# Performance work log

Measured on AMD Instinct MI355X. Metric: run time of the kernel, lower is better.

## Reference

```python
import jax, jax.numpy as jnp
import numpy as np

N = 50000      # nodes
E = 800000     # edges (before self-loops)
IN = 256
HID = 256
OUT = 128
D = 4
K = 4
K1 = 8
NUM_KS = K1 * ((1 << K) - 1)   # 120 centroids
S = HID // D                   # sub-dim per quantization slice
TAU = 1.0


def setup_inputs() -> dict:
    key = jax.random.key(0)
    ks = jax.random.split(key, 9)
    x = jax.random.normal(ks[0], (N, IN), jnp.float32)
    edge_index = jax.random.randint(ks[1], (2, E), 0, N, dtype=jnp.int64)
    def lin(k, fan_in, fan_out):
        return jax.random.normal(k, (fan_in, fan_out), jnp.float32) / np.float32(np.sqrt(fan_in))
    W0 = lin(ks[2], IN, HID); b0 = jnp.zeros((HID,), jnp.float32)
    W1 = lin(ks[3], HID, HID); b1 = jnp.zeros((HID,), jnp.float32)
    W2 = lin(ks[4], HID, OUT); b2 = jnp.zeros((OUT,), jnp.float32)
    # kaiming_normal on (NUM_KS, HID): std = sqrt(2 / fan_in), fan_in = HID
    centroids = jax.random.normal(ks[5], (NUM_KS, HID), jnp.float32) * np.float32(np.sqrt(2.0 / HID))
    return dict(x=x, edge_index=edge_index, W0=W0, b0=b0, W1=W1, b1=b1, W2=W2, b2=b2,
                centroids=centroids)


def gcn_conv(x, W, b, src, dst):
    # PyG GCNConv: add self-loops, symmetric normalization, aggregate at target
    n = x.shape[0]
    loops = jnp.arange(n, dtype=src.dtype)
    s2 = jnp.concatenate([src, loops])
    d2 = jnp.concatenate([dst, loops])
    deg = jax.ops.segment_sum(jnp.ones_like(d2, x.dtype), d2, num_segments=n)
    dinv = jnp.where(deg > 0, jax.lax.rsqrt(deg), 0.0)
    norm = dinv[s2] * dinv[d2]                      # [E+n]
    xw = x @ W                                      # [n, out]
    out = jax.ops.segment_sum(xw[s2] * norm[:, None], d2, num_segments=n)
    return out + b


def quantize(H, C):
    # H: [n, HID], C: [NUM_KS, HID]
    n = H.shape[0]
    Hr = H.reshape(n, D, S)
    Cr = C.reshape(NUM_KS, D, S)
    # products[n,k,d] = sum_s H[n,d,s] * C[k,d,s]
    prods = jnp.einsum('nds,kds->nkd', Hr, Cr) / TAU   # [n, NUM_KS, D]
    soft_l, hard_l, prob_l = [], [], []
    off = 0
    d_idx = jnp.arange(D)[None, :]
    for j in range(K):                 # K fixed small groups of sizes k_1<<j
        m = K1 << j
        sl = prods[:, off:off + m, :]                  # [n, m, D]
        p = jax.nn.softmax(sl, axis=1)                 # scatter_softmax within group
        Cg = Cr[off:off + m]                           # [m, D, S]
        soft_l.append(jnp.einsum('nmd,mds->nds', p, Cg))
        idx = jnp.argmax(sl, axis=1)                   # [n, D] scatter_max within group
        hard_l.append(Cg[idx, d_idx, :])               # [n, D, S]
        prob_l.append(p)
        off += m
    soft = jnp.stack(soft_l, 1).reshape(n, K, HID)
    hard = jnp.stack(hard_l, 1).reshape(n, K, HID)
    q = jax.lax.stop_gradient(hard - soft) + soft      # straight-through
    balance = jnp.concatenate(prob_l, 1).sum(0) / n    # [NUM_KS, D]
    k_blns = jnp.concatenate([jnp.full((K1 << j,), 1.0 / (K1 << j), jnp.float32) for j in range(K)])
    target = jnp.broadcast_to(k_blns[:, None], (NUM_KS, D))
    reg = jnp.linalg.norm(balance - target)
    pred = jnp.max(q, axis=1)                          # [n, HID]
    return pred, reg


def reference(x, edge_index, W0, b0, W1, b1, W2, b2, centroids):
    src, dst = edge_index[0], edge_index[1]
    h = jax.nn.leaky_relu(gcn_conv(x, W0, b0, src, dst), negative_slope=0.5)
    h = jax.nn.leaky_relu(gcn_conv(h, W1, b1, src, dst), negative_slope=0.5)
    pred, reg = quantize(h, centroids)
    h = h + pred
    out = gcn_conv(h, W2, b2, src, dst)
    return out, reg
```

## Files before the change

### kernel.cpp

```cpp
#include <hip/hip_runtime.h>
#include <math.h>



__global__ void k_init(int* cnt, int* cursor, int* counter, float* balance, int n) {
    int i = blockIdx.x * blockDim.x + threadIdx.x;
    if (i < n) { cnt[i] = 0; cursor[i] = 0; }
    if (i < 480) balance[i] = 0.f;
    if (i == 0) *counter = 0;
}

__global__ void k_count(const int* __restrict__ dst, int* __restrict__ cnt, int e) {
    int i = blockIdx.x * blockDim.x + threadIdx.x;
    if (i < e) atomicAdd(&cnt[dst[i]], 1);
}

__global__ void k_dinv(const int* __restrict__ cnt, float* __restrict__ dinv, int n) {
    int i = blockIdx.x * blockDim.x + threadIdx.x;
    if (i < n) dinv[i] = rsqrtf((float)cnt[i] + 1.0f);
}

__global__ void k_alloc(const int* __restrict__ cnt, int* __restrict__ row_start,
                        int* __restrict__ counter, int n) {
    int i = blockIdx.x * blockDim.x + threadIdx.x;
    if (i < n) row_start[i] = atomicAdd(counter, cnt[i]);
}

__global__ void k_fill(const int* __restrict__ src, const int* __restrict__ dst,
                       const float* __restrict__ dinv, const int* __restrict__ row_start,
                       int* __restrict__ cursor, int* __restrict__ csr_src,
                       float* __restrict__ csr_norm, int e) {
    int i = blockIdx.x * blockDim.x + threadIdx.x;
    if (i >= e) return;
    int s = src[i], d = dst[i];
    int slot = atomicAdd(&cursor[d], 1);
    int idx = row_start[d] + slot;
    csr_src[idx] = s;
    csr_norm[idx] = dinv[s] * dinv[d];
}


__global__ __launch_bounds__(256, 2) void k_gemm(const float* __restrict__ A,
                                                 const float* __restrict__ B,
                                                 float* __restrict__ C,
                                                 int M, int N, int K) {
    __shared__ float As[32][132];
    __shared__ float Bs[32][132];
    const int tid = threadIdx.x;
    const int bm = blockIdx.x * 128;
    const int bn = blockIdx.y * 128;
    const int tx = tid & 15, ty = tid >> 4;
    float acc[2][2][4][4] = {};

    for (int k0 = 0; k0 < K; k0 += 32) {
#pragma unroll
        for (int v = 0; v < 4; ++v) {
            int row = (tid >> 3) + v * 32;
            int col = (tid & 7) * 4;
            float4 a = make_float4(0.f, 0.f, 0.f, 0.f);
            if (bm + row < M) a = *(const float4*)(A + (size_t)(bm + row) * K + k0 + col);
            As[col + 0][row] = a.x;
            As[col + 1][row] = a.y;
            As[col + 2][row] = a.z;
            As[col + 3][row] = a.w;
        }
#pragma unroll
        for (int v = 0; v < 4; ++v) {
            int kr = (tid >> 5) + v * 8;
            int col = (tid & 31) * 4;
            *(float4*)&Bs[kr][col] = *(const float4*)(B + (size_t)(k0 + kr) * N + bn + col);
        }
        __syncthreads();
#pragma unroll
        for (int kk = 0; kk < 32; ++kk) {
            float4 a0 = *(float4*)&As[kk][ty * 4];
            float4 a1 = *(float4*)&As[kk][64 + ty * 4];
            float4 b0 = *(float4*)&Bs[kk][tx * 4];
            float4 b1 = *(float4*)&Bs[kk][64 + tx * 4];
            float av[2][4] = {{a0.x, a0.y, a0.z, a0.w}, {a1.x, a1.y, a1.z, a1.w}};
            float bv[2][4] = {{b0.x, b0.y, b0.z, b0.w}, {b1.x, b1.y, b1.z, b1.w}};
#pragma unroll
            for (int ri = 0; ri < 2; ++ri)
#pragma unroll
                for (int i = 0; i < 4; ++i)
#pragma unroll
                    for (int ci = 0; ci < 2; ++ci)
#pragma unroll
                        for (int j = 0; j < 4; ++j)
                            acc[ri][ci][i][j] += av[ri][i] * bv[ci][j];
        }
        __syncthreads();
    }
#pragma unroll
    for (int ri = 0; ri < 2; ++ri)
#pragma unroll
        for (int i = 0; i < 4; ++i) {
            int row = bm + ri * 64 + ty * 4 + i;
            if (row < M) {
#pragma unroll
                for (int ci = 0; ci < 2; ++ci) {
                    float4 o = make_float4(acc[ri][ci][i][0], acc[ri][ci][i][1],
                                           acc[ri][ci][i][2], acc[ri][ci][i][3]);
                    *(float4*)(C + (size_t)row * N + bn + ci * 64 + tx * 4) = o;
                }
            }
        }
}


template <bool RELU>
__global__ __launch_bounds__(256, 4) void k_agg4(const float* __restrict__ xw,
                                                 const float* __restrict__ dinv,
                                                 const int* __restrict__ csr_src,
                                                 const float* __restrict__ csr_norm,
                                                 const int* __restrict__ row_start,
                                                 const int* __restrict__ cnt,
                                                 const float* __restrict__ bias,
                                                 float* __restrict__ out, int n) {
    int node = blockIdx.x * 4 + (threadIdx.x >> 6);
    if (node >= n) return;
    int lane = threadIdx.x & 63;
    int c = lane * 4;
    float di = dinv[node];
    float4 self = *(const float4*)(xw + (size_t)node * 256 + c);
    float4 bv = *(const float4*)(bias + c);
    float sw = di * di;
    float ax = self.x * sw + bv.x;
    float ay = self.y * sw + bv.y;
    float az = self.z * sw + bv.z;
    float aw = self.w * sw + bv.w;
    int st = row_start[node];
    int m = cnt[node];
    for (int t0 = 0; t0 < m; t0 += 64) {
        int rem = m - t0;
        int cnt_i = rem < 64 ? rem : 64;
        int idx_l = 0;
        float nrm_l = 0.f;
        if (lane < cnt_i) {
            idx_l = csr_src[st + t0 + lane];
            nrm_l = csr_norm[st + t0 + lane];
        }
        int t = 0;
        for (; t + 8 <= cnt_i; t += 8) {
            const float* p0 = xw + (size_t)__shfl(idx_l, t + 0, 64) * 256 + c;
            const float* p1 = xw + (size_t)__shfl(idx_l, t + 1, 64) * 256 + c;
            const float* p2 = xw + (size_t)__shfl(idx_l, t + 2, 64) * 256 + c;
            const float* p3 = xw + (size_t)__shfl(idx_l, t + 3, 64) * 256 + c;
            const float* p4 = xw + (size_t)__shfl(idx_l, t + 4, 64) * 256 + c;
            const float* p5 = xw + (size_t)__shfl(idx_l, t + 5, 64) * 256 + c;
            const float* p6 = xw + (size_t)__shfl(idx_l, t + 6, 64) * 256 + c;
            const float* p7 = xw + (size_t)__shfl(idx_l, t + 7, 64) * 256 + c;
            float4 v0 = *(const float4*)p0;
            float4 v1 = *(const float4*)p1;
            float4 v2 = *(const float4*)p2;
            float4 v3 = *(const float4*)p3;
            float4 v4 = *(const float4*)p4;
            float4 v5 = *(const float4*)p5;
            float4 v6 = *(const float4*)p6;
            float4 v7 = *(const float4*)p7;
            float w0 = __shfl(nrm_l, t + 0, 64);
            float w1 = __shfl(nrm_l, t + 1, 64);
            float w2 = __shfl(nrm_l, t + 2, 64);
            float w3 = __shfl(nrm_l, t + 3, 64);
            float w4 = __shfl(nrm_l, t + 4, 64);
            float w5 = __shfl(nrm_l, t + 5, 64);
            float w6 = __shfl(nrm_l, t + 6, 64);
            float w7 = __shfl(nrm_l, t + 7, 64);
            ax += v0.x * w0; ay += v0.y * w0; az += v0.z * w0; aw += v0.w * w0;
            ax += v1.x * w1; ay += v1.y * w1; az += v1.z * w1; aw += v1.w * w1;
            ax += v2.x * w2; ay += v2.y * w2; az += v2.z * w2; aw += v2.w * w2;
            ax += v3.x * w3; ay += v3.y * w3; az += v3.z * w3; aw += v3.w * w3;
            ax += v4.x * w4; ay += v4.y * w4; az += v4.z * w4; aw += v4.w * w4;
            ax += v5.x * w5; ay += v5.y * w5; az += v5.z * w5; aw += v5.w * w5;
            ax += v6.x * w6; ay += v6.y * w6; az += v6.z * w6; aw += v6.w * w6;
            ax += v7.x * w7; ay += v7.y * w7; az += v7.z * w7; aw += v7.w * w7;
        }
        for (; t < cnt_i; ++t) {
            int s = __shfl(idx_l, t, 64);
            float w = __shfl(nrm_l, t, 64);
            float4 v = *(const float4*)(xw + (size_t)s * 256 + c);
            ax += v.x * w; ay += v.y * w; az += v.z * w; aw += v.w * w;
        }
    }
    if (RELU) {
        ax = ax > 0.f ? ax : 0.5f * ax;
        ay = ay > 0.f ? ay : 0.5f * ay;
        az = az > 0.f ? az : 0.5f * az;
        aw = aw > 0.f ? aw : 0.5f * aw;
    }
    *(float4*)(out + (size_t)node * 256 + c) = make_float4(ax, ay, az, aw);
}

__global__ __launch_bounds__(256, 4) void k_agg2(const float* __restrict__ xw,
                                                 const float* __restrict__ dinv,
                                                 const int* __restrict__ csr_src,
                                                 const float* __restrict__ csr_norm,
                                                 const int* __restrict__ row_start,
                                                 const int* __restrict__ cnt,
                                                 const float* __restrict__ bias,
                                                 float* __restrict__ out, int n) {
    int node = blockIdx.x * 4 + (threadIdx.x >> 6);
    if (node >= n) return;
    int lane = threadIdx.x & 63;
    int c = lane * 2;
    float di = dinv[node];
    float2 self = *(const float2*)(xw + (size_t)node * 128 + c);
    float2 bv = *(const float2*)(bias + c);
    float sw = di * di;
    float ax = self.x * sw + bv.x;
    float ay = self.y * sw + bv.y;
    int st = row_start[node];
    int m = cnt[node];
    for (int t0 = 0; t0 < m; t0 += 64) {
        int rem = m - t0;
        int cnt_i = rem < 64 ? rem : 64;
        int idx_l = 0;
        float nrm_l = 0.f;
        if (lane < cnt_i) {
            idx_l = csr_src[st + t0 + lane];
            nrm_l = csr_norm[st + t0 + lane];
        }
        int t = 0;
        for (; t + 8 <= cnt_i; t += 8) {
            const float* p0 = xw + (size_t)__shfl(idx_l, t + 0, 64) * 128 + c;
            const float* p1 = xw + (size_t)__shfl(idx_l, t + 1, 64) * 128 + c;
            const float* p2 = xw + (size_t)__shfl(idx_l, t + 2, 64) * 128 + c;
            const float* p3 = xw + (size_t)__shfl(idx_l, t + 3, 64) * 128 + c;
            const float* p4 = xw + (size_t)__shfl(idx_l, t + 4, 64) * 128 + c;
            const float* p5 = xw + (size_t)__shfl(idx_l, t + 5, 64) * 128 + c;
            const float* p6 = xw + (size_t)__shfl(idx_l, t + 6, 64) * 128 + c;
            const float* p7 = xw + (size_t)__shfl(idx_l, t + 7, 64) * 128 + c;
            float2 v0 = *(const float2*)p0;
            float2 v1 = *(const float2*)p1;
            float2 v2 = *(const float2*)p2;
            float2 v3 = *(const float2*)p3;
            float2 v4 = *(const float2*)p4;
            float2 v5 = *(const float2*)p5;
            float2 v6 = *(const float2*)p6;
            float2 v7 = *(const float2*)p7;
            float w0 = __shfl(nrm_l, t + 0, 64);
            float w1 = __shfl(nrm_l, t + 1, 64);
            float w2 = __shfl(nrm_l, t + 2, 64);
            float w3 = __shfl(nrm_l, t + 3, 64);
            float w4 = __shfl(nrm_l, t + 4, 64);
            float w5 = __shfl(nrm_l, t + 5, 64);
            float w6 = __shfl(nrm_l, t + 6, 64);
            float w7 = __shfl(nrm_l, t + 7, 64);
            ax += v0.x * w0; ay += v0.y * w0;
            ax += v1.x * w1; ay += v1.y * w1;
            ax += v2.x * w2; ay += v2.y * w2;
            ax += v3.x * w3; ay += v3.y * w3;
            ax += v4.x * w4; ay += v4.y * w4;
            ax += v5.x * w5; ay += v5.y * w5;
            ax += v6.x * w6; ay += v6.y * w6;
            ax += v7.x * w7; ay += v7.y * w7;
        }
        for (; t < cnt_i; ++t) {
            int s = __shfl(idx_l, t, 64);
            float w = __shfl(nrm_l, t, 64);
            float2 v = *(const float2*)(xw + (size_t)s * 128 + c);
            ax += v.x * w; ay += v.y * w;
        }
    }
    *(float2*)(out + (size_t)node * 128 + c) = make_float2(ax, ay);
}


__global__ __launch_bounds__(256, 4) void k_quant4(const float* __restrict__ h2,
                                                   const float* __restrict__ cent,
                                                   float* __restrict__ h3,
                                                   float* __restrict__ balance_g, int n) {
    __shared__ float As[32 * 132];
    __shared__ float Bs[32 * 132];
    __shared__ float bal4[4 * 128];
    __shared__ int km_ls[128 * 4];
    const int tid = threadIdx.x;
    const int n0 = blockIdx.x * 128;
    const int d = blockIdx.y;
    const int ty = tid >> 4, tx = tid & 15;
    const int wave = tid >> 6, lane = tid & 63;

    int gid, base, sz;
    if (tx == 0)       { gid = 0; base = 0;  sz = 1; }
    else if (tx <= 2)  { gid = 1; base = 1;  sz = 2; }
    else if (tx <= 6)  { gid = 2; base = 3;  sz = 4; }
    else if (tx <= 14) { gid = 3; base = 7;  sz = 8; }
    else               { gid = 0; base = 15; sz = 0; }
    const int l = tx - base;
    const int segbase = lane & 48;

    {
        int k = tid >> 3, r = tid & 7;
        int col = (r < 4) ? (60 + r) : (120 + r);
        Bs[k * 132 + col] = 0.f;
    }

    float acc[8][8] = {};
    for (int c0 = 0; c0 < 64; c0 += 32) {
#pragma unroll
        for (int it = 0; it < 4; ++it) {
            int q = it * 256 + tid;
            int row = q >> 3, k4 = q & 7;
            float4 v = make_float4(0.f, 0.f, 0.f, 0.f);
            if (n0 + row < n)
                v = *(const float4*)(h2 + (size_t)(n0 + row) * 256 + d * 64 + c0 + k4 * 4);
            As[(k4 * 4 + 0) * 132 + row] = v.x;
            As[(k4 * 4 + 1) * 132 + row] = v.y;
            As[(k4 * 4 + 2) * 132 + row] = v.z;
            As[(k4 * 4 + 3) * 132 + row] = v.w;
        }
#pragma unroll
        for (int it = 0; it < 4; ++it) {
            int q = it * 256 + tid;
            if (q < 960) {
                int c = q >> 3, k4 = q & 7;
                float4 v = *(const float4*)(cent + (size_t)c * 256 + d * 64 + c0 + k4 * 4);
                int col = ((c >> 3) << 2) + (((c >> 2) & 1) << 6) + (c & 3);
                Bs[(k4 * 4 + 0) * 132 + col] = v.x;
                Bs[(k4 * 4 + 1) * 132 + col] = v.y;
                Bs[(k4 * 4 + 2) * 132 + col] = v.z;
                Bs[(k4 * 4 + 3) * 132 + col] = v.w;
            }
        }
        __syncthreads();
#pragma unroll 4
        for (int k = 0; k < 32; ++k) {
            float4 a0 = *(const float4*)&As[k * 132 + ty * 8];
            float4 a1 = *(const float4*)&As[k * 132 + ty * 8 + 4];
            float4 b0 = *(const float4*)&Bs[k * 132 + tx * 4];
            float4 b1 = *(const float4*)&Bs[k * 132 + 64 + tx * 4];
            float av[8] = {a0.x, a0.y, a0.z, a0.w, a1.x, a1.y, a1.z, a1.w};
            float bv[8] = {b0.x, b0.y, b0.z, b0.w, b1.x, b1.y, b1.z, b1.w};
#pragma unroll
            for (int i = 0; i < 8; ++i)
#pragma unroll
                for (int j = 0; j < 8; ++j)
                    acc[i][j] += av[i] * bv[j];
        }
        __syncthreads();
    }

    float balp[8] = {};
#pragma unroll
    for (int i = 0; i < 8; ++i) {
        const int node = ty * 8 + i;
        const bool act = (n0 + node) < n;
        float m = acc[i][0];
        int am = tx * 8;
#pragma unroll
        for (int j = 1; j < 8; ++j)
            if (acc[i][j] > m) { m = acc[i][j]; am = tx * 8 + j; }
#pragma unroll
        for (int s = 1; s <= 4; s <<= 1) {
            int pl = l ^ s;
            int srcl = segbase + base + pl;
            float mo = __shfl(m, srcl, 64);
            int amo = __shfl(am, srcl, 64);
            if (pl < sz && (mo > m || (mo == m && amo < am))) { m = mo; am = amo; }
        }
        float Z = 0.f;
#pragma unroll
        for (int j = 0; j < 8; ++j) {
            float e2 = expf(acc[i][j] - m);
            acc[i][j] = e2;
            Z += e2;
        }
#pragma unroll
        for (int s = 1; s <= 4; s <<= 1) {
            int pl = l ^ s;
            int srcl = segbase + base + pl;
            float Zo = __shfl(Z, srcl, 64);
            if (pl < sz) Z += Zo;
        }
        float invZ = (act && sz > 0) ? (1.0f / Z) : 0.f;
#pragma unroll
        for (int j = 0; j < 8; ++j) balp[j] += acc[i][j] * invZ;
        if (l == 0 && sz > 0) km_ls[node * 4 + gid] = am;
    }

#pragma unroll
    for (int j = 0; j < 8; ++j) {
        float v = balp[j];
        v += __shfl_xor(v, 16, 64);
        v += __shfl_xor(v, 32, 64);
        balp[j] = v;
    }
    if (lane < 16) {
#pragma unroll
        for (int j = 0; j < 8; ++j)
            bal4[wave * 128 + tx * 8 + j] = balp[j];
    }
    __syncthreads();
    if (tid < 120) {
        float s = bal4[tid] + bal4[128 + tid] + bal4[256 + tid] + bal4[384 + tid];
        atomicAdd(&balance_g[tid * 4 + d], s);
    }

    {
        const int node = tid >> 1;
        const int half = tid & 1;
        if (n0 + node < n) {
            int k0 = km_ls[node * 4 + 0], k1 = km_ls[node * 4 + 1];
            int k2 = km_ls[node * 4 + 2], k3 = km_ls[node * 4 + 3];
            const float* hp = h2 + (size_t)(n0 + node) * 256 + d * 64 + half * 32;
            const float* c0 = cent + (size_t)k0 * 256 + d * 64 + half * 32;
            const float* c1 = cent + (size_t)k1 * 256 + d * 64 + half * 32;
            const float* c2 = cent + (size_t)k2 * 256 + d * 64 + half * 32;
            const float* c3 = cent + (size_t)k3 * 256 + d * 64 + half * 32;
            float* op = h3 + (size_t)(n0 + node) * 256 + d * 64 + half * 32;
#pragma unroll
            for (int q = 0; q < 8; ++q) {
                int g = q * 4;
                float4 hv = *(const float4*)(hp + g);
                float4 v0 = *(const float4*)(c0 + g);
                float4 v1 = *(const float4*)(c1 + g);
                float4 v2 = *(const float4*)(c2 + g);
                float4 v3 = *(const float4*)(c3 + g);
                float4 r;
                r.x = hv.x + fmaxf(fmaxf(v0.x, v1.x), fmaxf(v2.x, v3.x));
                r.y = hv.y + fmaxf(fmaxf(v0.y, v1.y), fmaxf(v2.y, v3.y));
                r.z = hv.z + fmaxf(fmaxf(v0.z, v1.z), fmaxf(v2.z, v3.z));
                r.w = hv.w + fmaxf(fmaxf(v0.w, v1.w), fmaxf(v2.w, v3.w));
                *(float4*)(op + g) = r;
            }
        }
    }
}

__global__ void k_reg(const float* __restrict__ balance_g, float* __restrict__ out_reg,
                      float inv_n) {
    __shared__ float red[512];
    int tid = threadIdx.x;
    float v = 0.f;
    if (tid < 480) {
        int k = tid >> 2;
        float target = (k < 8) ? 0.125f : (k < 24) ? 0.0625f : (k < 56) ? 0.03125f : 0.015625f;
        float b = balance_g[tid] * inv_n;
        float df = b - target;
        v = df * df;
    }
    red[tid] = v;
    __syncthreads();
    for (int s = 256; s > 0; s >>= 1) {
        if (tid < s) red[tid] += red[tid + s];
        __syncthreads();
    }
    if (tid == 0) *out_reg = sqrtf(red[0]);
}


extern "C" void kernel_launch(void* const* d_in, const int* in_sizes, int n_in,
                              void* d_out, int out_size, void* d_ws, size_t ws_size,
                              hipStream_t stream) {
    const float* x    = (const float*)d_in[0];
    const int*   ei   = (const int*)d_in[1];
    const float* W0   = (const float*)d_in[2];
    const float* b0   = (const float*)d_in[3];
    const float* W1   = (const float*)d_in[4];
    const float* b1   = (const float*)d_in[5];
    const float* W2   = (const float*)d_in[6];
    const float* b2   = (const float*)d_in[7];
    const float* cent = (const float*)d_in[8];
    const int n = in_sizes[0] / 256;
    const int e = in_sizes[1] / 2;
    const int* src = ei;
    const int* dst = ei + e;
    float* out = (float*)d_out;

    char* w = (char*)d_ws;
    float* bufA = (float*)w;      w += (size_t)n * 256 * 4;
    float* bufB = (float*)w;      w += (size_t)n * 256 * 4;
    float* dinv = (float*)w;      w += (size_t)n * 4;
    int* cnt = (int*)w;           w += (size_t)n * 4;
    int* row_start = (int*)w;     w += (size_t)n * 4;
    int* cursor = (int*)w;        w += (size_t)n * 4;
    int* csr_src = (int*)w;       w += (size_t)e * 4;
    float* csr_norm = (float*)w;  w += (size_t)e * 4;
    int* counter = (int*)w;       w += 256;
    float* balance = (float*)w;   w += 480 * 4;

    const int tb = 256;
    k_init<<<(n + tb - 1) / tb, tb, 0, stream>>>(cnt, cursor, counter, balance, n);
    k_count<<<(e + tb - 1) / tb, tb, 0, stream>>>(dst, cnt, e);
    k_dinv<<<(n + tb - 1) / tb, tb, 0, stream>>>(cnt, dinv, n);
    k_alloc<<<(n + tb - 1) / tb, tb, 0, stream>>>(cnt, row_start, counter, n);
    k_fill<<<(e + tb - 1) / tb, tb, 0, stream>>>(src, dst, dinv, row_start, cursor,
                                                 csr_src, csr_norm, e);

    dim3 g1((n + 127) / 128, 2);
    k_gemm<<<g1, 256, 0, stream>>>(x, W0, bufA, n, 256, 256);
    k_agg4<true><<<(n + 3) / 4, 256, 0, stream>>>(bufA, dinv, csr_src, csr_norm,
                                                  row_start, cnt, b0, bufB, n);
    k_gemm<<<g1, 256, 0, stream>>>(bufB, W1, bufA, n, 256, 256);
    k_agg4<true><<<(n + 3) / 4, 256, 0, stream>>>(bufA, dinv, csr_src, csr_norm,
                                                  row_start, cnt, b1, bufB, n);

    dim3 gq((n + 127) / 128, 4);
    k_quant4<<<gq, 256, 0, stream>>>(bufB, cent, bufA, balance, n);

    dim3 g3((n + 127) / 128, 1);
    k_gemm<<<g3, 256, 0, stream>>>(bufA, W2, bufB, n, 128, 256);
    k_agg2<<<(n + 3) / 4, 256, 0, stream>>>(bufB, dinv, csr_src, csr_norm,
                                            row_start, cnt, b2, out, n);
    k_reg<<<1, 512, 0, stream>>>(balance, out + (size_t)n * 128, 1.0f / (float)n);
}
```

Before: 747.0 us.

## Replace FP32 SIMT GEMM with split-bf16 MFMA GEMM (3-pass hi/lo)

Swaps the scalar FP32 register-tiled GEMM for one built on bf16 MFMA instructions. Each FP32 operand is split into high and low bf16 halves and three MFMA passes (lo*hi, hi*lo, hi*hi) approximate FP32 accuracy. The aim is to move the three dense layers' matmul work onto the matrix cores. The cost is extra conversion work when staging tiles into shared memory, scattered 2-byte writes for the transposed B tile, scalar output stores, and slightly lower precision than true FP32.

```diff
diff --git a/kernel.cpp b/kernel.cpp
--- a/kernel.cpp
+++ b/kernel.cpp
@@ -40,71 +40,107 @@
 }
 
 
-__global__ __launch_bounds__(256, 2) void k_gemm(const float* __restrict__ A,
-                                                 const float* __restrict__ B,
-                                                 float* __restrict__ C,
-                                                 int M, int N, int K) {
-    __shared__ float As[32][132];
-    __shared__ float Bs[32][132];
+typedef short bf16x8 __attribute__((ext_vector_type(8)));
+typedef float f32x4 __attribute__((ext_vector_type(4)));
+
+__device__ __forceinline__ unsigned short bf16_rne(float a) {
+    unsigned u = __builtin_bit_cast(unsigned, a);
+    return (unsigned short)((u + 0x7FFFu + ((u >> 16) & 1u)) >> 16);
+}
+__device__ __forceinline__ float bf16_to_f(unsigned short h) {
+    return __builtin_bit_cast(float, (unsigned)h << 16);
+}
+
+__global__ __launch_bounds__(256, 3) void k_gemm_mfma(const float* __restrict__ A,
+                                                      const float* __restrict__ B,
+                                                      float* __restrict__ C,
+                                                      int M, int N) {
+    constexpr int K = 256;
+    __shared__ unsigned short Ash[128 * 40];
+    __shared__ unsigned short Asl[128 * 40];
+    __shared__ unsigned short Bsh[128 * 40];
+    __shared__ unsigned short Bsl[128 * 40];
     const int tid = threadIdx.x;
     const int bm = blockIdx.x * 128;
     const int bn = blockIdx.y * 128;
-    const int tx = tid & 15, ty = tid >> 4;
-    float acc[2][2][4][4] = {};
+    const int wave = tid >> 6, lane = tid & 63;
+    const int wr = wave >> 1, wc = wave & 1;
+    const int lr = lane & 15, lk = lane >> 4;
+
+    f32x4 acc[4][4] = {};
 
     for (int k0 = 0; k0 < K; k0 += 32) {
 #pragma unroll
-        for (int v = 0; v < 4; ++v) {
-            int row = (tid >> 3) + v * 32;
-            int col = (tid & 7) * 4;
-            float4 a = make_float4(0.f, 0.f, 0.f, 0.f);
-            if (bm + row < M) a = *(const float4*)(A + (size_t)(bm + row) * K + k0 + col);
-            As[col + 0][row] = a.x;
-            As[col + 1][row] = a.y;
-            As[col + 2][row] = a.z;
-            As[col + 3][row] = a.w;
-        }
-#pragma unroll
-        for (int v = 0; v < 4; ++v) {
-            int kr = (tid >> 5) + v * 8;
-            int col = (tid & 31) * 4;
-            *(float4*)&Bs[kr][col] = *(const float4*)(B + (size_t)(k0 + kr) * N + bn + col);
+        for (int it = 0; it < 4; ++it) {
+            int q = it * 256 + tid;
+            int row = q >> 3, kq = q & 7;
+            float4 v = make_float4(0.f, 0.f, 0.f, 0.f);
+            if (bm + row < M) v = *(const float4*)(A + (size_t)(bm + row) * K + k0 + kq * 4);
+            float e[4] = {v.x, v.y, v.z, v.w};
+            unsigned hh[4], ll[4];
+#pragma unroll
+            for (int t = 0; t < 4; ++t) {
+                unsigned short h = bf16_rne(e[t]);
+                unsigned short l = bf16_rne(e[t] - bf16_to_f(h));
+                hh[t] = h; ll[t] = l;
+            }
+            unsigned off = row * 40 + kq * 4;
+            *(uint2*)&Ash[off] = make_uint2(hh[0] | (hh[1] << 16), hh[2] | (hh[3] << 16));
+            *(uint2*)&Asl[off] = make_uint2(ll[0] | (ll[1] << 16), ll[2] | (ll[3] << 16));
+        }
+#pragma unroll
+        for (int it = 0; it < 4; ++it) {
+            int q = it * 256 + tid;
+            int k = q >> 5, nq = q & 31;
+            float4 v = *(const float4*)(B + (size_t)(k0 + k) * N + bn + nq * 4);
+            float e[4] = {v.x, v.y, v.z, v.w};
+#pragma unroll
+            for (int t = 0; t < 4; ++t) {
+                unsigned short h = bf16_rne(e[t]);
+                unsigned short l = bf16_rne(e[t] - bf16_to_f(h));
+                Bsh[(nq * 4 + t) * 40 + k] = h;
+                Bsl[(nq * 4 + t) * 40 + k] = l;
+            }
         }
         __syncthreads();
-#pragma unroll
-        for (int kk = 0; kk < 32; ++kk) {
-            float4 a0 = *(float4*)&As[kk][ty * 4];
-            float4 a1 = *(float4*)&As[kk][64 + ty * 4];
-            float4 b0 = *(float4*)&Bs[kk][tx * 4];
-            float4 b1 = *(float4*)&Bs[kk][64 + tx * 4];
-            float av[2][4] = {{a0.x, a0.y, a0.z, a0.w}, {a1.x, a1.y, a1.z, a1.w}};
-            float bv[2][4] = {{b0.x, b0.y, b0.z, b0.w}, {b1.x, b1.y, b1.z, b1.w}};
-#pragma unroll
-            for (int ri = 0; ri < 2; ++ri)
-#pragma unroll
-                for (int i = 0; i < 4; ++i)
-#pragma unroll
-                    for (int ci = 0; ci < 2; ++ci)
-#pragma unroll
-                        for (int j = 0; j < 4; ++j)
-                            acc[ri][ci][i][j] += av[ri][i] * bv[ci][j];
-        }
+
+        bf16x8 ah[4], al[4], bh[4], bl[4];
+#pragma unroll
+        for (int i = 0; i < 4; ++i) {
+            unsigned off = (wr * 64 + i * 16 + lr) * 40 + lk * 8;
+            ah[i] = *(bf16x8*)&Ash[off];
+            al[i] = *(bf16x8*)&Asl[off];
+        }
+#pragma unroll
+        for (int j = 0; j < 4; ++j) {
+            unsigned off = (wc * 64 + j * 16 + lr) * 40 + lk * 8;
+            bh[j] = *(bf16x8*)&Bsh[off];
+            bl[j] = *(bf16x8*)&Bsl[off];
+        }
+#pragma unroll
+        for (int i = 0; i < 4; ++i)
+#pragma unroll
+            for (int j = 0; j < 4; ++j) {
+                acc[i][j] = __builtin_amdgcn_mfma_f32_16x16x32_bf16(al[i], bh[j], acc[i][j], 0, 0, 0);
+                acc[i][j] = __builtin_amdgcn_mfma_f32_16x16x32_bf16(ah[i], bl[j], acc[i][j], 0, 0, 0);
+                acc[i][j] = __builtin_amdgcn_mfma_f32_16x16x32_bf16(ah[i], bh[j], acc[i][j], 0, 0, 0);
+            }
         __syncthreads();
     }
-#pragma unroll
-    for (int ri = 0; ri < 2; ++ri)
-#pragma unroll
-        for (int i = 0; i < 4; ++i) {
-            int row = bm + ri * 64 + ty * 4 + i;
+
+#pragma unroll
+    for (int i = 0; i < 4; ++i) {
+        int rbase = bm + wr * 64 + i * 16 + lk * 4;
+#pragma unroll
+        for (int r = 0; r < 4; ++r) {
+            int row = rbase + r;
             if (row < M) {
 #pragma unroll
-                for (int ci = 0; ci < 2; ++ci) {
-                    float4 o = make_float4(acc[ri][ci][i][0], acc[ri][ci][i][1],
-                                           acc[ri][ci][i][2], acc[ri][ci][i][3]);
-                    *(float4*)(C + (size_t)row * N + bn + ci * 64 + tx * 4) = o;
-                }
+                for (int j = 0; j < 4; ++j)
+                    C[(size_t)row * N + bn + wc * 64 + j * 16 + lr] = acc[i][j][r];
             }
         }
+    }
 }
 
 
@@ -488,10 +524,10 @@
                                                  csr_src, csr_norm, e);
 
     dim3 g1((n + 127) / 128, 2);
-    k_gemm<<<g1, 256, 0, stream>>>(x, W0, bufA, n, 256, 256);
+    k_gemm_mfma<<<g1, 256, 0, stream>>>(x, W0, bufA, n, 256);
     k_agg4<true><<<(n + 3) / 4, 256, 0, stream>>>(bufA, dinv, csr_src, csr_norm,
                                                   row_start, cnt, b0, bufB, n);
-    k_gemm<<<g1, 256, 0, stream>>>(bufB, W1, bufA, n, 256, 256);
+    k_gemm_mfma<<<g1, 256, 0, stream>>>(bufB, W1, bufA, n, 256);
     k_agg4<true><<<(n + 3) / 4, 256, 0, stream>>>(bufA, dinv, csr_src, csr_norm,
                                                   row_start, cnt, b1, bufB, n);
 
@@ -499,7 +535,7 @@
     k_quant4<<<gq, 256, 0, stream>>>(bufB, cent, bufA, balance, n);
 
     dim3 g3((n + 127) / 128, 1);
-    k_gemm<<<g3, 256, 0, stream>>>(bufA, W2, bufB, n, 128, 256);
+    k_gemm_mfma<<<g3, 256, 0, stream>>>(bufA, W2, bufB, n, 128);
     k_agg2<<<(n + 3) / 4, 256, 0, stream>>>(bufB, dinv, csr_src, csr_norm,
                                             row_start, cnt, b2, out, n);
     k_reg<<<1, 512, 0, stream>>>(balance, out + (size_t)n * 128, 1.0f / (float)n);
```

Result: faster. 723.7 us (-3.1%).
